# Kernel optimization log

Hardware: AMD Instinct MI355X
Metric: run time of the kernel (lower is better)

The kernel has to match this reference:

```python
import jax, jax.numpy as jnp
import numpy as np

B, S, D = 2, 1024, 768
H, HD = 12, 64
E, K, F = 8, 2, 3072
EPS = 1e-5


def _ln(x, g, b):
    mu = jnp.mean(x, -1, keepdims=True)
    var = jnp.mean(jnp.square(x - mu), -1, keepdims=True)
    return (x - mu) * jax.lax.rsqrt(var + EPS) * g + b


def setup_inputs() -> dict:
    key = jax.random.key(0)
    ks = jax.random.split(key, 12)
    s = lambda k, shape, sc: jax.random.normal(k, shape, jnp.float32) * sc
    return {
        "hidden_states": s(ks[0], (B, S, D), 1.0),
        "ln1_g": jnp.ones((D,), jnp.float32), "ln1_b": jnp.zeros((D,), jnp.float32),
        "w_attn": s(ks[1], (D, 3 * D), 0.02), "b_attn": jnp.zeros((3 * D,), jnp.float32),
        "w_attnproj": s(ks[2], (D, D), 0.02), "b_attnproj": jnp.zeros((D,), jnp.float32),
        "ln2_g": jnp.ones((D,), jnp.float32), "ln2_b": jnp.zeros((D,), jnp.float32),
        "w_router": s(ks[3], (E, D), 0.01),
        "w_fc": s(ks[4], (E, D, F), 0.02 / E), "b_fc": jnp.zeros((E, F), jnp.float32),
        "w_proj": s(ks[5], (E, F, D), 0.02 / E), "b_proj": jnp.zeros((E, D), jnp.float32),
    }


def reference(hidden_states, ln1_g, ln1_b, w_attn, b_attn, w_attnproj, b_attnproj,
              ln2_g, ln2_b, w_router, w_fc, b_fc, w_proj, b_proj):
    # --- attention sub-block (GPT-2 style, causal) ---
    residual = hidden_states
    x = _ln(hidden_states, ln1_g, ln1_b)
    qkv = x @ w_attn + b_attn                         # [B,S,3D]
    q, k, v = jnp.split(qkv, 3, axis=-1)
    def heads(t):
        return t.reshape(B, S, H, HD).transpose(0, 2, 1, 3)  # [B,H,S,HD]
    q, k, v = heads(q), heads(k), heads(v)
    scores = jnp.einsum("bhqd,bhkd->bhqk", q, k) / np.sqrt(HD).astype(np.float32)
    causal = jnp.tril(jnp.ones((S, S), bool))
    scores = jnp.where(causal, scores, jnp.finfo(scores.dtype).min)
    attn = jax.nn.softmax(scores, axis=-1)
    ctx = jnp.einsum("bhqk,bhkd->bhqd", attn, v)
    ctx = ctx.transpose(0, 2, 1, 3).reshape(B, S, D)
    attn_out = ctx @ w_attnproj + b_attnproj
    hs = attn_out + residual

    # --- MoE FFN sub-block ---
    residual = hs
    x2 = _ln(hs, ln2_g, ln2_b)
    logits = x2 @ w_router.T                          # [B,S,E]
    probs = jax.nn.softmax(logits, axis=-1)
    top_w, top_idx = jax.lax.top_k(probs, K)          # [B,S,K]
    top_w = top_w / jnp.sum(top_w, -1, keepdims=True)
    gates = jnp.sum(jax.nn.one_hot(top_idx, E, dtype=x2.dtype) * top_w[..., None], axis=2)  # [B,S,E]
    h = jax.nn.gelu(jnp.einsum("bsd,edf->bsef", x2, w_fc) + b_fc, approximate=False)
    y = jnp.einsum("bsef,efd->bsed", h, w_proj) + b_proj
    moe_out = jnp.einsum("bse,bsed->bsd", gates, y)
    return moe_out + residual
```

## Files before the change

### kernel.cpp

```cpp
#include <hip/hip_runtime.h>
#include <hip/hip_bf16.h>
#include <math.h>

#define NB 2
#define SEQ 1024
#define DM 768
#define NHEAD 12
#define HDIM 64
#define NEXP 8
#define FF 3072
#define NTOK (NB*SEQ)
#define TDIM (3*DM)
#define LNEPS 1e-5f
#define NSLOT (NTOK*2)

typedef __attribute__((ext_vector_type(8))) short v8s;
typedef __attribute__((ext_vector_type(4))) float v4f;

#define GLDS16(src, dst) \
    __builtin_amdgcn_global_load_lds((const __attribute__((address_space(1))) unsigned int*)(src), \
                                     (__attribute__((address_space(3))) unsigned int*)(dst), 16, 0, 0)

#define BARF() do { asm volatile("" ::: "memory"); __builtin_amdgcn_s_barrier(); asm volatile("" ::: "memory"); } while(0)
#define WAITV(n) asm volatile("s_waitcnt vmcnt(" #n ")" ::: "memory")

static __device__ __forceinline__ float bf2f(unsigned short u){
    return __uint_as_float(((unsigned)u) << 16);
}
static __device__ __forceinline__ unsigned short f2bf(float f){
    unsigned u = __float_as_uint(f);
    u += 0x7fffu + ((u >> 16) & 1u);
    return (unsigned short)(u >> 16);
}
static __device__ __forceinline__ float gelu_exact(float x){
    return 0.5f * x * (1.0f + erff(x * 0.70710678118654752440f));
}

__global__ __launch_bounds__(256) void tconv_kernel(const float* __restrict__ in,
                                                    unsigned short* __restrict__ out,
                                                    int R, int C){
    __shared__ float T[32][33];
    size_t base = (size_t)blockIdx.z * R * C;
    int c0 = blockIdx.x * 32, r0 = blockIdx.y * 32;
    int t = threadIdx.x;
    int tr = t >> 3, tc4 = (t & 7) * 4;
    float4 v = *(const float4*)&in[base + (size_t)(r0 + tr) * C + c0 + tc4];
    T[tr][tc4+0] = v.x; T[tr][tc4+1] = v.y; T[tr][tc4+2] = v.z; T[tr][tc4+3] = v.w;
    __syncthreads();
    int oc = t >> 3, or4 = (t & 7) * 4;
    ushort4 o;
    o.x = f2bf(T[or4+0][oc]); o.y = f2bf(T[or4+1][oc]);
    o.z = f2bf(T[or4+2][oc]); o.w = f2bf(T[or4+3][oc]);
    *(ushort4*)&out[base + (size_t)(c0 + oc) * R + r0 + or4] = o;
}

__global__ __launch_bounds__(256) void ln_b(const float* __restrict__ in,
                                            const float* __restrict__ g,
                                            const float* __restrict__ b,
                                            unsigned short* __restrict__ outb){
    int t = blockIdx.x;
    const float* row = in + (size_t)t * DM;
    int tid = threadIdx.x;
    float v0 = row[tid], v1 = row[tid + 256], v2 = row[tid + 512];
    float s  = v0 + v1 + v2;
    float ss = v0*v0 + v1*v1 + v2*v2;
    for (int off = 32; off; off >>= 1){
        s  += __shfl_down(s, off);
        ss += __shfl_down(ss, off);
    }
    __shared__ float ls[4], lss[4];
    int wid = tid >> 6, lane = tid & 63;
    if (lane == 0){ ls[wid] = s; lss[wid] = ss; }
    __syncthreads();
    if (tid == 0){
        float a = ls[0] + ls[1] + ls[2] + ls[3];
        float c = lss[0] + lss[1] + lss[2] + lss[3];
        float mu = a / (float)DM;
        float var = c / (float)DM - mu * mu;
        ls[0] = mu; lss[0] = rsqrtf(var + LNEPS);
    }
    __syncthreads();
    float mu = ls[0], rs = lss[0];
    unsigned short* obrow = outb + (size_t)t * DM;
    obrow[tid]     = f2bf((v0 - mu) * rs * g[tid]       + b[tid]);
    obrow[tid+256] = f2bf((v1 - mu) * rs * g[tid + 256] + b[tid + 256]);
    obrow[tid+512] = f2bf((v2 - mu) * rs * g[tid + 512] + b[tid + 512]);
}

__global__ __launch_bounds__(256) void ln_router(const float* __restrict__ in,
                                                 const float* __restrict__ g,
                                                 const float* __restrict__ b,
                                                 const float* __restrict__ wr,
                                                 unsigned short* __restrict__ outb,
                                                 int* __restrict__ cnt,
                                                 int* __restrict__ expTok,
                                                 int* __restrict__ tokE,
                                                 int* __restrict__ tokPos,
                                                 float* __restrict__ tokGate){
    int t = blockIdx.x;
    const float* row = in + (size_t)t * DM;
    int tid = threadIdx.x;
    float v0 = row[tid], v1 = row[tid + 256], v2 = row[tid + 512];
    float s  = v0 + v1 + v2;
    float ss = v0*v0 + v1*v1 + v2*v2;
    for (int off = 32; off; off >>= 1){
        s  += __shfl_down(s, off);
        ss += __shfl_down(ss, off);
    }
    __shared__ float ls[4], lss[4];
    __shared__ float wsum[4][NEXP];
    int wid = tid >> 6, lane = tid & 63;
    if (lane == 0){ ls[wid] = s; lss[wid] = ss; }
    __syncthreads();
    if (tid == 0){
        float a = ls[0] + ls[1] + ls[2] + ls[3];
        float c = lss[0] + lss[1] + lss[2] + lss[3];
        float mu = a / (float)DM;
        float var = c / (float)DM - mu * mu;
        ls[0] = mu; lss[0] = rsqrtf(var + LNEPS);
    }
    __syncthreads();
    float mu = ls[0], rs = lss[0];
    float o0 = (v0 - mu) * rs * g[tid]       + b[tid];
    float o1 = (v1 - mu) * rs * g[tid + 256] + b[tid + 256];
    float o2 = (v2 - mu) * rs * g[tid + 512] + b[tid + 512];
    unsigned short* obrow = outb + (size_t)t * DM;
    obrow[tid] = f2bf(o0); obrow[tid+256] = f2bf(o1); obrow[tid+512] = f2bf(o2);
    float p[NEXP];
    #pragma unroll
    for (int e = 0; e < NEXP; e++)
        p[e] = o0*wr[e*DM + tid] + o1*wr[e*DM + tid + 256] + o2*wr[e*DM + tid + 512];
    #pragma unroll
    for (int e = 0; e < NEXP; e++)
        for (int off = 32; off; off >>= 1) p[e] += __shfl_down(p[e], off);
    if (lane == 0){
        #pragma unroll
        for (int e = 0; e < NEXP; e++) wsum[wid][e] = p[e];
    }
    __syncthreads();
    if (tid == 0){
        float lg[NEXP];
        #pragma unroll
        for (int e = 0; e < NEXP; e++)
            lg[e] = wsum[0][e] + wsum[1][e] + wsum[2][e] + wsum[3][e];
        int i0 = 0; float m0 = lg[0];
        #pragma unroll
        for (int e = 1; e < NEXP; e++) if (lg[e] > m0){ m0 = lg[e]; i0 = e; }
        int i1 = -1; float m1 = -INFINITY;
        #pragma unroll
        for (int e = 0; e < NEXP; e++) if (e != i0 && lg[e] > m1){ m1 = lg[e]; i1 = e; }
        float mx = fmaxf(m0, m1);
        float e0 = __expf(m0 - mx), e1 = __expf(m1 - mx);
        float inv = 1.0f / (e0 + e1);
        int p0 = atomicAdd(&cnt[i0], 1);
        int p1 = atomicAdd(&cnt[i1], 1);
        expTok[i0*NTOK + p0] = t;
        expTok[i1*NTOK + p1] = t;
        tokE[t*2]   = i0; tokE[t*2+1]   = i1;
        tokPos[t*2] = p0; tokPos[t*2+1] = p1;
        tokGate[t*2]   = e0 * inv;
        tokGate[t*2+1] = e1 * inv;
    }
}

__global__ __launch_bounds__(256) void mm_qkv(const unsigned short* __restrict__ Ab,
                                              const unsigned short* __restrict__ Bb,
                                              const float* __restrict__ bias,
                                              unsigned short* __restrict__ Qb,
                                              unsigned short* __restrict__ Kb,
                                              unsigned short* __restrict__ Vt){
    __shared__ __align__(16) unsigned short As[4][64*32];
    __shared__ __align__(16) unsigned short Bs[4][128*32];
    int bm = blockIdx.y * 64, bn = blockIdx.x * 128;
    int tid = threadIdx.x, wave = tid >> 6, lane = tid & 63;
    int quad = lane >> 4, l15 = lane & 15;
    int wm = wave >> 1, wn = wave & 1;
    int lrow = lane >> 2, lchunk = (lane & 3) * 8;
    const unsigned short* aS  = Ab + (size_t)(bm +      wave*16 + lrow) * DM + lchunk;
    const unsigned short* bS0 = Bb + (size_t)(bn +      wave*16 + lrow) * DM + lchunk;
    const unsigned short* bS1 = Bb + (size_t)(bn + 64 + wave*16 + lrow) * DM + lchunk;
    v4f acc[2][4];
    #pragma unroll
    for (int i = 0; i < 2; i++)
        #pragma unroll
        for (int j = 0; j < 4; j++) acc[i][j] = (v4f){0.f,0.f,0.f,0.f};

#define QKV_STAGE(buf, kt) do { int kb = (kt)*32; \
    GLDS16(aS  + kb, &As[buf][(wave*16)*32]); \
    GLDS16(bS0 + kb, &Bs[buf][(     wave*16)*32]); \
    GLDS16(bS1 + kb, &Bs[buf][(64 + wave*16)*32]); \
} while(0)
#define QKV_COMP(buf) do { \
    v8s a[2], bfr[4]; \
    _Pragma("unroll") \
    for (int i = 0; i < 2; i++) a[i] = *(const v8s*)&As[buf][(wm*32 + i*16 + l15)*32 + quad*8]; \
    _Pragma("unroll") \
    for (int i = 0; i < 4; i++) bfr[i] = *(const v8s*)&Bs[buf][(wn*64 + i*16 + l15)*32 + quad*8]; \
    _Pragma("unroll") \
    for (int mi = 0; mi < 2; mi++) \
        _Pragma("unroll") \
        for (int ni = 0; ni < 4; ni++) \
            acc[mi][ni] = __builtin_amdgcn_mfma_f32_16x16x32_bf16(a[mi], bfr[ni], acc[mi][ni], 0, 0, 0); \
} while(0)

    const int NK = DM/32;
    QKV_STAGE(0, 0); QKV_STAGE(1, 1); QKV_STAGE(2, 2);
    #pragma unroll 1
    for (int kt = 0; kt < NK; kt++){
        int rem = NK - kt;
        if (rem > 3){ QKV_STAGE((kt+3)&3, kt+3); WAITV(9); }
        else if (rem == 3){ WAITV(6); }
        else if (rem == 2){ WAITV(3); }
        else { WAITV(0); }
        BARF();
        QKV_COMP(kt&3);
        BARF();
    }
    int btyp = bn / DM;
    #pragma unroll
    for (int ni = 0; ni < 4; ni++){
        int n = bn + wn*64 + ni*16 + l15;
        float bb = bias[n];
        int hd = n % DM; int h = hd >> 6; int d = hd & 63;
        #pragma unroll
        for (int mi = 0; mi < 2; mi++){
            int m = bm + wm*32 + mi*16 + quad*4;
            int b = m >> 10, sd = m & 1023;
            size_t bhbase = (size_t)(b*NHEAD + h);
            if (btyp == 0){
                #pragma unroll
                for (int r = 0; r < 4; r++)
                    Qb[(bhbase*SEQ + sd + r)*HDIM + d] = f2bf((acc[mi][ni][r] + bb) * 0.125f);
            } else if (btyp == 1){
                #pragma unroll
                for (int r = 0; r < 4; r++)
                    Kb[(bhbase*SEQ + sd + r)*HDIM + d] = f2bf(acc[mi][ni][r] + bb);
            } else {
                ushort4 o;
                o.x = f2bf(acc[mi][ni][0] + bb); o.y = f2bf(acc[mi][ni][1] + bb);
                o.z = f2bf(acc[mi][ni][2] + bb); o.w = f2bf(acc[mi][ni][3] + bb);
                *(ushort4*)&Vt[(bhbase*HDIM + d)*SEQ + sd] = o;
            }
        }
    }
}

__global__ __launch_bounds__(64) void fattn(const unsigned short* __restrict__ Qb,
                                            const unsigned short* __restrict__ Kb,
                                            const unsigned short* __restrict__ Vt,
                                            unsigned short* __restrict__ ctxb){
    int bh = blockIdx.x >> 5;
    int q0 = (31 - (blockIdx.x & 31)) * 32;
    int h = bh % NHEAD, b = bh / NHEAD;
    int lane = threadIdx.x;
    int quad = lane >> 4, l15 = lane & 15;

    __shared__ __align__(16) unsigned short Plds[32*32];

    const unsigned short* qp = Qb + ((size_t)bh*SEQ + q0 + l15) * HDIM + quad*8;
    v8s qa00 = *(const v8s*)qp;
    v8s qa01 = *(const v8s*)(qp + 32);
    v8s qa10 = *(const v8s*)(qp + 16*HDIM);
    v8s qa11 = *(const v8s*)(qp + 16*HDIM + 32);

    v4f o[2][4];
    #pragma unroll
    for (int i = 0; i < 2; i++)
        #pragma unroll
        for (int j = 0; j < 4; j++) o[i][j] = (v4f){0.f,0.f,0.f,0.f};
    float mrow[2][4], lrow[2][4];
    #pragma unroll
    for (int i = 0; i < 2; i++)
        #pragma unroll
        for (int r = 0; r < 4; r++){ mrow[i][r] = -1e30f; lrow[i][r] = 0.f; }

    int nch = (q0 >> 5) + 1;
    for (int ch = 0; ch < nch; ch++){
        int kt = ch * 32;
        const unsigned short* kp = Kb + ((size_t)bh*SEQ + kt + l15) * HDIM + quad*8;
        v8s k00 = *(const v8s*)kp;
        v8s k01 = *(const v8s*)(kp + 32);
        v8s k10 = *(const v8s*)(kp + 16*HDIM);
        v8s k11 = *(const v8s*)(kp + 16*HDIM + 32);
        v4f s00 = {0,0,0,0}, s01 = {0,0,0,0}, s10 = {0,0,0,0}, s11 = {0,0,0,0};
        s00 = __builtin_amdgcn_mfma_f32_16x16x32_bf16(qa00, k00, s00, 0, 0, 0);
        s00 = __builtin_amdgcn_mfma_f32_16x16x32_bf16(qa01, k01, s00, 0, 0, 0);
        s01 = __builtin_amdgcn_mfma_f32_16x16x32_bf16(qa00, k10, s01, 0, 0, 0);
        s01 = __builtin_amdgcn_mfma_f32_16x16x32_bf16(qa01, k11, s01, 0, 0, 0);
        s10 = __builtin_amdgcn_mfma_f32_16x16x32_bf16(qa10, k00, s10, 0, 0, 0);
        s10 = __builtin_amdgcn_mfma_f32_16x16x32_bf16(qa11, k01, s10, 0, 0, 0);
        s11 = __builtin_amdgcn_mfma_f32_16x16x32_bf16(qa10, k10, s11, 0, 0, 0);
        s11 = __builtin_amdgcn_mfma_f32_16x16x32_bf16(qa11, k11, s11, 0, 0, 0);

        int key0 = kt + l15, key1 = kt + 16 + l15;
        float alpha[2][4];
        #pragma unroll
        for (int mi = 0; mi < 2; mi++){
            #pragma unroll
            for (int r = 0; r < 4; r++){
                int qrow = q0 + mi*16 + quad*4 + r;
                float sv0 = mi ? s10[r] : s00[r];
                float sv1 = mi ? s11[r] : s01[r];
                float v0 = (key0 <= qrow) ? sv0 : -1e30f;
                float v1 = (key1 <= qrow) ? sv1 : -1e30f;
                float mx = fmaxf(v0, v1);
                mx = fmaxf(mx, __shfl_xor(mx, 1));
                mx = fmaxf(mx, __shfl_xor(mx, 2));
                mx = fmaxf(mx, __shfl_xor(mx, 4));
                mx = fmaxf(mx, __shfl_xor(mx, 8));
                float mn = fmaxf(mrow[mi][r], mx);
                alpha[mi][r] = __expf(mrow[mi][r] - mn);
                float p0 = __expf(v0 - mn);
                float p1 = __expf(v1 - mn);
                float ps = p0 + p1;
                ps += __shfl_xor(ps, 1);
                ps += __shfl_xor(ps, 2);
                ps += __shfl_xor(ps, 4);
                ps += __shfl_xor(ps, 8);
                lrow[mi][r] = lrow[mi][r] * alpha[mi][r] + ps;
                mrow[mi][r] = mn;
                Plds[(mi*16 + quad*4 + r)*32 + l15]      = f2bf(p0);
                Plds[(mi*16 + quad*4 + r)*32 + 16 + l15] = f2bf(p1);
            }
        }
        #pragma unroll
        for (int mi = 0; mi < 2; mi++)
            #pragma unroll
            for (int df = 0; df < 4; df++)
                #pragma unroll
                for (int r = 0; r < 4; r++)
                    o[mi][df][r] *= alpha[mi][r];
        __syncthreads();
        v8s pa0 = *(const v8s*)&Plds[l15*32 + quad*8];
        v8s pa1 = *(const v8s*)&Plds[(16 + l15)*32 + quad*8];
        const unsigned short* vp = Vt + ((size_t)bh*HDIM + l15) * SEQ + kt + quad*8;
        #pragma unroll
        for (int df = 0; df < 4; df++){
            v8s vb = *(const v8s*)(vp + df*16*SEQ);
            o[0][df] = __builtin_amdgcn_mfma_f32_16x16x32_bf16(pa0, vb, o[0][df], 0, 0, 0);
            o[1][df] = __builtin_amdgcn_mfma_f32_16x16x32_bf16(pa1, vb, o[1][df], 0, 0, 0);
        }
        __syncthreads();
    }
    #pragma unroll
    for (int mi = 0; mi < 2; mi++){
        #pragma unroll
        for (int r = 0; r < 4; r++){
            float inv = 1.0f / lrow[mi][r];
            size_t orow = (size_t)(b*SEQ + q0 + mi*16 + quad*4 + r) * DM + h*HDIM;
            #pragma unroll
            for (int df = 0; df < 4; df++)
                ctxb[orow + df*16 + l15] = f2bf(o[mi][df][r] * inv);
        }
    }
}

__global__ __launch_bounds__(256) void mm_attnproj(const unsigned short* __restrict__ Ab,
                                                   const unsigned short* __restrict__ Bb,
                                                   const float* __restrict__ bias,
                                                   const float* __restrict__ res,
                                                   float* __restrict__ C){
    __shared__ __align__(16) unsigned short As[4][64*32];
    __shared__ __align__(16) unsigned short Bs[4][64*32];
    int bm = blockIdx.y * 64, bn = blockIdx.x * 64;
    int tid = threadIdx.x, wave = tid >> 6, lane = tid & 63;
    int quad = lane >> 4, l15 = lane & 15;
    int wm = wave >> 1, wn = wave & 1;
    int lrow = lane >> 2, lchunk = (lane & 3) * 8;
    const unsigned short* aS = Ab + (size_t)(bm + wave*16 + lrow) * DM + lchunk;
    const unsigned short* bS = Bb + (size_t)(bn + wave*16 + lrow) * DM + lchunk;
    v4f acc[2][2];
    #pragma unroll
    for (int i = 0; i < 2; i++)
        #pragma unroll
        for (int j = 0; j < 2; j++) acc[i][j] = (v4f){0.f,0.f,0.f,0.f};

#define AP_STAGE(buf, kt) do { int kb = (kt)*32; \
    GLDS16(aS + kb, &As[buf][(wave*16)*32]); \
    GLDS16(bS + kb, &Bs[buf][(wave*16)*32]); \
} while(0)
#define AP_COMP(buf) do { \
    v8s a[2], bfr[2]; \
    _Pragma("unroll") \
    for (int i = 0; i < 2; i++){ \
        a[i]   = *(const v8s*)&As[buf][(wm*32 + i*16 + l15)*32 + quad*8]; \
        bfr[i] = *(const v8s*)&Bs[buf][(wn*32 + i*16 + l15)*32 + quad*8]; \
    } \
    _Pragma("unroll") \
    for (int mi = 0; mi < 2; mi++) \
        _Pragma("unroll") \
        for (int ni = 0; ni < 2; ni++) \
            acc[mi][ni] = __builtin_amdgcn_mfma_f32_16x16x32_bf16(a[mi], bfr[ni], acc[mi][ni], 0, 0, 0); \
} while(0)

    const int NK = DM/32;
    AP_STAGE(0, 0); AP_STAGE(1, 1); AP_STAGE(2, 2);
    #pragma unroll 1
    for (int kt = 0; kt < NK; kt++){
        int rem = NK - kt;
        if (rem > 3){ AP_STAGE((kt+3)&3, kt+3); WAITV(6); }
        else if (rem == 3){ WAITV(4); }
        else if (rem == 2){ WAITV(2); }
        else { WAITV(0); }
        BARF();
        AP_COMP(kt&3);
        BARF();
    }
    #pragma unroll
    for (int ni = 0; ni < 2; ni++){
        int n = bn + wn*32 + ni*16 + l15;
        float bb = bias[n];
        #pragma unroll
        for (int mi = 0; mi < 2; mi++){
            int m = bm + wm*32 + mi*16 + quad*4;
            #pragma unroll
            for (int r = 0; r < 4; r++)
                C[(size_t)(m + r) * DM + n] = acc[mi][ni][r] + bb + res[(size_t)(m + r) * DM + n];
        }
    }
}

__global__ __launch_bounds__(256) void mm_fc(const unsigned short* __restrict__ Xb,
                                             const unsigned short* __restrict__ Wb,
                                             const float* __restrict__ bfc,
                                             const int* __restrict__ expTok,
                                             const int* __restrict__ cnt,
                                             const int* __restrict__ offE,
                                             unsigned short* __restrict__ H){
    int e = blockIdx.z, tile = blockIdx.y;
    int c = cnt[e];
    int rows = c - tile * 64;
    if (rows <= 0) return;
    __shared__ __align__(16) unsigned short As[4][64*32];
    __shared__ __align__(16) unsigned short Bs[4][128*32];
    __shared__ int toks[64];
    int bn = blockIdx.x * 128;
    int tid = threadIdx.x, wave = tid >> 6, lane = tid & 63;
    if (tid < 64){
        int idx = tile * 64 + tid;
        if (idx >= c) idx = c - 1;
        toks[tid] = expTok[e * NTOK + idx];
    }
    __syncthreads();
    int quad = lane >> 4, l15 = lane & 15;
    int wm = wave >> 1, wn = wave & 1;
    int lrow = lane >> 2, lchunk = (lane & 3) * 8;
    int tok0 = toks[wave*16 + lrow];
    const unsigned short* Be = Wb + (size_t)e * FF * DM;
    const unsigned short* aS  = Xb + (size_t)tok0 * DM + lchunk;
    const unsigned short* bS0 = Be + (size_t)(bn +      wave*16 + lrow) * DM + lchunk;
    const unsigned short* bS1 = Be + (size_t)(bn + 64 + wave*16 + lrow) * DM + lchunk;
    v4f acc[2][4];
    #pragma unroll
    for (int i = 0; i < 2; i++)
        #pragma unroll
        for (int j = 0; j < 4; j++) acc[i][j] = (v4f){0.f,0.f,0.f,0.f};

#define FC_STAGE(buf, kt) do { int kb = (kt)*32; \
    GLDS16(aS  + kb, &As[buf][(wave*16)*32]); \
    GLDS16(bS0 + kb, &Bs[buf][(     wave*16)*32]); \
    GLDS16(bS1 + kb, &Bs[buf][(64 + wave*16)*32]); \
} while(0)
#define FC_COMP(buf) do { \
    v8s a[2], bfr[4]; \
    _Pragma("unroll") \
    for (int i = 0; i < 2; i++) a[i] = *(const v8s*)&As[buf][(wm*32 + i*16 + l15)*32 + quad*8]; \
    _Pragma("unroll") \
    for (int i = 0; i < 4; i++) bfr[i] = *(const v8s*)&Bs[buf][(wn*64 + i*16 + l15)*32 + quad*8]; \
    _Pragma("unroll") \
    for (int mi = 0; mi < 2; mi++) \
        _Pragma("unroll") \
        for (int ni = 0; ni < 4; ni++) \
            acc[mi][ni] = __builtin_amdgcn_mfma_f32_16x16x32_bf16(a[mi], bfr[ni], acc[mi][ni], 0, 0, 0); \
} while(0)

    const int NK = DM/32;
    FC_STAGE(0, 0); FC_STAGE(1, 1); FC_STAGE(2, 2);
    #pragma unroll 1
    for (int kt = 0; kt < NK; kt++){
        int rem = NK - kt;
        if (rem > 3){ FC_STAGE((kt+3)&3, kt+3); WAITV(9); }
        else if (rem == 3){ WAITV(6); }
        else if (rem == 2){ WAITV(3); }
        else { WAITV(0); }
        BARF();
        FC_COMP(kt&3);
        BARF();
    }
    int slot0 = offE[e] + tile * 64;
    #pragma unroll
    for (int ni = 0; ni < 4; ni++){
        int n = bn + wn*64 + ni*16 + l15;
        float bb = bfc[(size_t)e * FF + n];
        #pragma unroll
        for (int mi = 0; mi < 2; mi++){
            int ml = wm*32 + mi*16 + quad*4;
            #pragma unroll
            for (int r = 0; r < 4; r++)
                if (ml + r < rows)
                    H[(size_t)(slot0 + ml + r) * FF + n] = f2bf(gelu_exact(acc[mi][ni][r] + bb));
        }
    }
}

__global__ __launch_bounds__(256) void mm_proj(const unsigned short* __restrict__ H,
                                               const unsigned short* __restrict__ Wb,
                                               const int* __restrict__ cnt,
                                               const int* __restrict__ offE,
                                               float* __restrict__ Yp){
    int e = blockIdx.z, tile = blockIdx.y;
    int c = cnt[e];
    int rows = c - tile * 64;
    if (rows <= 0) return;
    int sk = blockIdx.x & 1;
    int bn = (blockIdx.x >> 1) * 128;
    __shared__ __align__(16) unsigned short As[4][64*32];
    __shared__ __align__(16) unsigned short Bs[4][128*32];
    int tid = threadIdx.x, wave = tid >> 6, lane = tid & 63;
    int quad = lane >> 4, l15 = lane & 15;
    int wm = wave >> 1, wn = wave & 1;
    int slot0 = offE[e] + tile * 64;
    int lrow = lane >> 2, lchunk = (lane & 3) * 8;
    int arow = wave*16 + lrow;
    int arl = arow < rows ? arow : rows - 1;
    const unsigned short* Be = Wb + (size_t)e * DM * FF;
    const unsigned short* aS  = H  + (size_t)(slot0 + arl) * FF + sk*1536 + lchunk;
    const unsigned short* bS0 = Be + (size_t)(bn +      wave*16 + lrow) * FF + sk*1536 + lchunk;
    const unsigned short* bS1 = Be + (size_t)(bn + 64 + wave*16 + lrow) * FF + sk*1536 + lchunk;
    v4f acc[2][4];
    #pragma unroll
    for (int i = 0; i < 2; i++)
        #pragma unroll
        for (int j = 0; j < 4; j++) acc[i][j] = (v4f){0.f,0.f,0.f,0.f};

#define PJ_STAGE(buf, kt) do { int kb = (kt)*32; \
    GLDS16(aS  + kb, &As[buf][(wave*16)*32]); \
    GLDS16(bS0 + kb, &Bs[buf][(     wave*16)*32]); \
    GLDS16(bS1 + kb, &Bs[buf][(64 + wave*16)*32]); \
} while(0)
#define PJ_COMP(buf) do { \
    v8s a[2], bfr[4]; \
    _Pragma("unroll") \
    for (int i = 0; i < 2; i++) a[i] = *(const v8s*)&As[buf][(wm*32 + i*16 + l15)*32 + quad*8]; \
    _Pragma("unroll") \
    for (int i = 0; i < 4; i++) bfr[i] = *(const v8s*)&Bs[buf][(wn*64 + i*16 + l15)*32 + quad*8]; \
    _Pragma("unroll") \
    for (int mi = 0; mi < 2; mi++) \
        _Pragma("unroll") \
        for (int ni = 0; ni < 4; ni++) \
            acc[mi][ni] = __builtin_amdgcn_mfma_f32_16x16x32_bf16(a[mi], bfr[ni], acc[mi][ni], 0, 0, 0); \
} while(0)

    const int NK = 1536/32;
    PJ_STAGE(0, 0); PJ_STAGE(1, 1); PJ_STAGE(2, 2);
    #pragma unroll 1
    for (int kt = 0; kt < NK; kt++){
        int rem = NK - kt;
        if (rem > 3){ PJ_STAGE((kt+3)&3, kt+3); WAITV(9); }
        else if (rem == 3){ WAITV(6); }
        else if (rem == 2){ WAITV(3); }
        else { WAITV(0); }
        BARF();
        PJ_COMP(kt&3);
        BARF();
    }
    float* Yo = Yp + (size_t)sk * NSLOT * DM;
    #pragma unroll
    for (int ni = 0; ni < 4; ni++){
        int n = bn + wn*64 + ni*16 + l15;
        #pragma unroll
        for (int mi = 0; mi < 2; mi++){
            int ml = wm*32 + mi*16 + quad*4;
            #pragma unroll
            for (int r = 0; r < 4; r++)
                if (ml + r < rows)
                    Yo[(size_t)(slot0 + ml + r) * DM + n] = acc[mi][ni][r];
        }
    }
}

__global__ void offsets_kernel(const int* __restrict__ cnt, int* __restrict__ offE){
    if (threadIdx.x == 0 && blockIdx.x == 0){
        int a = 0;
        for (int e = 0; e < NEXP; e++){ offE[e] = a; a += cnt[e]; }
    }
}

__global__ __launch_bounds__(256) void combine_kernel(const float* __restrict__ hs,
                                                      const float* __restrict__ Yp,
                                                      const float* __restrict__ bproj,
                                                      const int* __restrict__ tokE,
                                                      const int* __restrict__ tokPos,
                                                      const float* __restrict__ tokGate,
                                                      const int* __restrict__ offE,
                                                      float* __restrict__ out){
    int t = blockIdx.x;
    int e0 = tokE[t*2], e1 = tokE[t*2+1];
    int s0 = offE[e0] + tokPos[t*2];
    int s1 = offE[e1] + tokPos[t*2+1];
    float g0 = tokGate[t*2], g1 = tokGate[t*2+1];
    const float* y0a = Yp + (size_t)s0 * DM;
    const float* y0b = Yp + (size_t)NSLOT * DM + (size_t)s0 * DM;
    const float* y1a = Yp + (size_t)s1 * DM;
    const float* y1b = Yp + (size_t)NSLOT * DM + (size_t)s1 * DM;
    const float* b0 = bproj + (size_t)e0 * DM;
    const float* b1 = bproj + (size_t)e1 * DM;
    const float* hr = hs + (size_t)t * DM;
    float* orow = out + (size_t)t * DM;
    for (int d = threadIdx.x; d < DM; d += 256){
        orow[d] = hr[d] + g0 * (y0a[d] + y0b[d] + b0[d]) + g1 * (y1a[d] + y1b[d] + b1[d]);
    }
}

extern "C" void kernel_launch(void* const* d_in, const int* in_sizes, int n_in,
                              void* d_out, int out_size, void* d_ws, size_t ws_size,
                              hipStream_t stream){
    (void)in_sizes; (void)n_in; (void)out_size; (void)ws_size;
    const float* hidden  = (const float*)d_in[0];
    const float* ln1_g   = (const float*)d_in[1];
    const float* ln1_b   = (const float*)d_in[2];
    const float* w_attn  = (const float*)d_in[3];
    const float* b_attn  = (const float*)d_in[4];
    const float* w_aproj = (const float*)d_in[5];
    const float* b_aproj = (const float*)d_in[6];
    const float* ln2_g   = (const float*)d_in[7];
    const float* ln2_b   = (const float*)d_in[8];
    const float* w_rout  = (const float*)d_in[9];
    const float* w_fc    = (const float*)d_in[10];
    const float* b_fc    = (const float*)d_in[11];
    const float* w_proj  = (const float*)d_in[12];
    const float* b_proj  = (const float*)d_in[13];
    float* out = (float*)d_out;

    char* ws = (char*)d_ws;
    float*          hs   = (float*)(ws + 0);
    unsigned short* xb   = (unsigned short*)(ws + 6291456);
    unsigned short* Qb   = (unsigned short*)(ws + 9437184);
    unsigned short* Kb   = (unsigned short*)(ws + 12582912);
    unsigned short* Vt   = (unsigned short*)(ws + 15728640);
    unsigned short* ctxb = (unsigned short*)(ws + 18874368);
    unsigned short* Wab  = (unsigned short*)(ws + 22020096);
    unsigned short* Wapb = (unsigned short*)(ws + 25559040);
    unsigned short* H    = (unsigned short*)(ws + 9437184);
    unsigned short* Wfcb = (unsigned short*)(ws + 34603008);
    unsigned short* Wprb = (unsigned short*)(ws + 72351744);
    float*          Yp   = (float*)(ws + 34603008);
    char* rt = ws + 110100480;
    int* cnt      = (int*)(rt + 0);
    int* offE     = (int*)(rt + 64);
    int* expTok   = (int*)(rt + 128);
    int* tokE     = (int*)(rt + 128 + 65536);
    int* tokPos   = (int*)(rt + 128 + 81920);
    float* tokGate= (float*)(rt + 128 + 98304);

    hipMemsetAsync(cnt, 0, NEXP * sizeof(int), stream);

    tconv_kernel<<<dim3(TDIM/32, DM/32, 1), 256, 0, stream>>>(w_attn, Wab, DM, TDIM);
    tconv_kernel<<<dim3(DM/32, DM/32, 1), 256, 0, stream>>>(w_aproj, Wapb, DM, DM);
    tconv_kernel<<<dim3(FF/32, DM/32, NEXP), 256, 0, stream>>>(w_fc, Wfcb, DM, FF);
    tconv_kernel<<<dim3(DM/32, FF/32, NEXP), 256, 0, stream>>>(w_proj, Wprb, FF, DM);

    ln_b<<<NTOK, 256, 0, stream>>>(hidden, ln1_g, ln1_b, xb);
    mm_qkv<<<dim3(TDIM/128, NTOK/64), 256, 0, stream>>>(xb, Wab, b_attn, Qb, Kb, Vt);
    fattn<<<NB*NHEAD*32, 64, 0, stream>>>(Qb, Kb, Vt, ctxb);
    mm_attnproj<<<dim3(DM/64, NTOK/64), 256, 0, stream>>>(ctxb, Wapb, b_aproj, hidden, hs);
    ln_router<<<NTOK, 256, 0, stream>>>(hs, ln2_g, ln2_b, w_rout, xb,
                                        cnt, expTok, tokE, tokPos, tokGate);
    offsets_kernel<<<1, 64, 0, stream>>>(cnt, offE);
    mm_fc<<<dim3(FF/128, NTOK/64, NEXP), 256, 0, stream>>>(xb, Wfcb, b_fc, expTok, cnt, offE, H);
    mm_proj<<<dim3((DM/128)*2, NTOK/64, NEXP), 256, 0, stream>>>(H, Wprb, cnt, offE, Yp);
    combine_kernel<<<NTOK, 256, 0, stream>>>(hs, Yp, b_proj, tokE, tokPos, tokGate, offE, out);
}
```

Measured before the change: 493.0 us.

## Shrink QKV and proj GEMM tiles to 64x64 and use double buffering

The QKV and MoE down-projection GEMMs go from 64x128 to 64x64 output tiles, which doubles their grid size. All three GEMMs (QKV, FC, proj) drop the 4-stage global-to-LDS prefetch pipeline for 2-stage double buffering. The goal is to cut LDS use per block so more blocks fit on each CU, and to expose more parallelism in the smaller GEMMs. The cost is shallower latency hiding and less operand reuse per tile.

```diff
diff --git a/kernel.cpp b/kernel.cpp
--- a/kernel.cpp
+++ b/kernel.cpp
@@ -169,57 +169,53 @@
                                               unsigned short* __restrict__ Qb,
                                               unsigned short* __restrict__ Kb,
                                               unsigned short* __restrict__ Vt){
-    __shared__ __align__(16) unsigned short As[4][64*32];
-    __shared__ __align__(16) unsigned short Bs[4][128*32];
-    int bm = blockIdx.y * 64, bn = blockIdx.x * 128;
+    __shared__ __align__(16) unsigned short As[2][64*32];
+    __shared__ __align__(16) unsigned short Bs[2][64*32];
+    int bm = blockIdx.y * 64, bn = blockIdx.x * 64;
     int tid = threadIdx.x, wave = tid >> 6, lane = tid & 63;
     int quad = lane >> 4, l15 = lane & 15;
     int wm = wave >> 1, wn = wave & 1;
-    int lrow = lane >> 2, lchunk = (lane & 3) * 8;
-    const unsigned short* aS  = Ab + (size_t)(bm +      wave*16 + lrow) * DM + lchunk;
-    const unsigned short* bS0 = Bb + (size_t)(bn +      wave*16 + lrow) * DM + lchunk;
-    const unsigned short* bS1 = Bb + (size_t)(bn + 64 + wave*16 + lrow) * DM + lchunk;
-    v4f acc[2][4];
+    int arow = tid >> 2, achunk = (tid & 3) * 8;
+    const unsigned short* aS = Ab + (size_t)(bm + arow) * DM + achunk;
+    const unsigned short* bS = Bb + (size_t)(bn + arow) * DM + achunk;
+    v4f acc[2][2];
     #pragma unroll
     for (int i = 0; i < 2; i++)
         #pragma unroll
-        for (int j = 0; j < 4; j++) acc[i][j] = (v4f){0.f,0.f,0.f,0.f};
+        for (int j = 0; j < 2; j++) acc[i][j] = (v4f){0.f,0.f,0.f,0.f};
 
 #define QKV_STAGE(buf, kt) do { int kb = (kt)*32; \
-    GLDS16(aS  + kb, &As[buf][(wave*16)*32]); \
-    GLDS16(bS0 + kb, &Bs[buf][(     wave*16)*32]); \
-    GLDS16(bS1 + kb, &Bs[buf][(64 + wave*16)*32]); \
+    GLDS16(aS + kb, &As[buf][(wave*16)*32]); \
+    GLDS16(bS + kb, &Bs[buf][(wave*16)*32]); \
 } while(0)
 #define QKV_COMP(buf) do { \
-    v8s a[2], bfr[4]; \
-    _Pragma("unroll") \
-    for (int i = 0; i < 2; i++) a[i] = *(const v8s*)&As[buf][(wm*32 + i*16 + l15)*32 + quad*8]; \
-    _Pragma("unroll") \
-    for (int i = 0; i < 4; i++) bfr[i] = *(const v8s*)&Bs[buf][(wn*64 + i*16 + l15)*32 + quad*8]; \
+    v8s a[2], bfr[2]; \
+    _Pragma("unroll") \
+    for (int i = 0; i < 2; i++){ \
+        a[i]   = *(const v8s*)&As[buf][(wm*32 + i*16 + l15)*32 + quad*8]; \
+        bfr[i] = *(const v8s*)&Bs[buf][(wn*32 + i*16 + l15)*32 + quad*8]; \
+    } \
     _Pragma("unroll") \
     for (int mi = 0; mi < 2; mi++) \
         _Pragma("unroll") \
-        for (int ni = 0; ni < 4; ni++) \
+        for (int ni = 0; ni < 2; ni++) \
             acc[mi][ni] = __builtin_amdgcn_mfma_f32_16x16x32_bf16(a[mi], bfr[ni], acc[mi][ni], 0, 0, 0); \
 } while(0)
 
     const int NK = DM/32;
-    QKV_STAGE(0, 0); QKV_STAGE(1, 1); QKV_STAGE(2, 2);
+    QKV_STAGE(0, 0);
     #pragma unroll 1
     for (int kt = 0; kt < NK; kt++){
-        int rem = NK - kt;
-        if (rem > 3){ QKV_STAGE((kt+3)&3, kt+3); WAITV(9); }
-        else if (rem == 3){ WAITV(6); }
-        else if (rem == 2){ WAITV(3); }
-        else { WAITV(0); }
-        BARF();
-        QKV_COMP(kt&3);
+        if (NK - kt > 1){ QKV_STAGE((kt+1)&1, kt+1); WAITV(2); }
+        else            { WAITV(0); }
+        BARF();
+        QKV_COMP(kt&1);
         BARF();
     }
     int btyp = bn / DM;
     #pragma unroll
-    for (int ni = 0; ni < 4; ni++){
-        int n = bn + wn*64 + ni*16 + l15;
+    for (int ni = 0; ni < 2; ni++){
+        int n = bn + wn*32 + ni*16 + l15;
         float bb = bias[n];
         int hd = n % DM; int h = hd >> 6; int d = hd & 63;
         #pragma unroll
@@ -431,8 +427,8 @@
     int c = cnt[e];
     int rows = c - tile * 64;
     if (rows <= 0) return;
-    __shared__ __align__(16) unsigned short As[4][64*32];
-    __shared__ __align__(16) unsigned short Bs[4][128*32];
+    __shared__ __align__(16) unsigned short As[2][64*32];
+    __shared__ __align__(16) unsigned short Bs[2][128*32];
     __shared__ int toks[64];
     int bn = blockIdx.x * 128;
     int tid = threadIdx.x, wave = tid >> 6, lane = tid & 63;
@@ -475,16 +471,13 @@
 } while(0)
 
     const int NK = DM/32;
-    FC_STAGE(0, 0); FC_STAGE(1, 1); FC_STAGE(2, 2);
+    FC_STAGE(0, 0);
     #pragma unroll 1
     for (int kt = 0; kt < NK; kt++){
-        int rem = NK - kt;
-        if (rem > 3){ FC_STAGE((kt+3)&3, kt+3); WAITV(9); }
-        else if (rem == 3){ WAITV(6); }
-        else if (rem == 2){ WAITV(3); }
-        else { WAITV(0); }
-        BARF();
-        FC_COMP(kt&3);
+        if (NK - kt > 1){ FC_STAGE((kt+1)&1, kt+1); WAITV(3); }
+        else            { WAITV(0); }
+        BARF();
+        FC_COMP(kt&1);
         BARF();
     }
     int slot0 = offE[e] + tile * 64;
@@ -513,61 +506,56 @@
     int rows = c - tile * 64;
     if (rows <= 0) return;
     int sk = blockIdx.x & 1;
-    int bn = (blockIdx.x >> 1) * 128;
-    __shared__ __align__(16) unsigned short As[4][64*32];
-    __shared__ __align__(16) unsigned short Bs[4][128*32];
+    int bn = (blockIdx.x >> 1) * 64;
+    __shared__ __align__(16) unsigned short As[2][64*32];
+    __shared__ __align__(16) unsigned short Bs[2][64*32];
     int tid = threadIdx.x, wave = tid >> 6, lane = tid & 63;
     int quad = lane >> 4, l15 = lane & 15;
     int wm = wave >> 1, wn = wave & 1;
     int slot0 = offE[e] + tile * 64;
-    int lrow = lane >> 2, lchunk = (lane & 3) * 8;
-    int arow = wave*16 + lrow;
+    int arow = tid >> 2, achunk = (tid & 3) * 8;
     int arl = arow < rows ? arow : rows - 1;
     const unsigned short* Be = Wb + (size_t)e * DM * FF;
-    const unsigned short* aS  = H  + (size_t)(slot0 + arl) * FF + sk*1536 + lchunk;
-    const unsigned short* bS0 = Be + (size_t)(bn +      wave*16 + lrow) * FF + sk*1536 + lchunk;
-    const unsigned short* bS1 = Be + (size_t)(bn + 64 + wave*16 + lrow) * FF + sk*1536 + lchunk;
-    v4f acc[2][4];
+    const unsigned short* aS = H  + (size_t)(slot0 + arl) * FF + sk*1536 + achunk;
+    const unsigned short* bS = Be + (size_t)(bn + arow) * FF + sk*1536 + achunk;
+    v4f acc[2][2];
     #pragma unroll
     for (int i = 0; i < 2; i++)
         #pragma unroll
-        for (int j = 0; j < 4; j++) acc[i][j] = (v4f){0.f,0.f,0.f,0.f};
+        for (int j = 0; j < 2; j++) acc[i][j] = (v4f){0.f,0.f,0.f,0.f};
 
 #define PJ_STAGE(buf, kt) do { int kb = (kt)*32; \
-    GLDS16(aS  + kb, &As[buf][(wave*16)*32]); \
-    GLDS16(bS0 + kb, &Bs[buf][(     wave*16)*32]); \
-    GLDS16(bS1 + kb, &Bs[buf][(64 + wave*16)*32]); \
+    GLDS16(aS + kb, &As[buf][(wave*16)*32]); \
+    GLDS16(bS + kb, &Bs[buf][(wave*16)*32]); \
 } while(0)
 #define PJ_COMP(buf) do { \
-    v8s a[2], bfr[4]; \
-    _Pragma("unroll") \
-    for (int i = 0; i < 2; i++) a[i] = *(const v8s*)&As[buf][(wm*32 + i*16 + l15)*32 + quad*8]; \
-    _Pragma("unroll") \
-    for (int i = 0; i < 4; i++) bfr[i] = *(const v8s*)&Bs[buf][(wn*64 + i*16 + l15)*32 + quad*8]; \
+    v8s a[2], bfr[2]; \
+    _Pragma("unroll") \
+    for (int i = 0; i < 2; i++){ \
+        a[i]   = *(const v8s*)&As[buf][(wm*32 + i*16 + l15)*32 + quad*8]; \
+        bfr[i] = *(const v8s*)&Bs[buf][(wn*32 + i*16 + l15)*32 + quad*8]; \
+    } \
     _Pragma("unroll") \
     for (int mi = 0; mi < 2; mi++) \
         _Pragma("unroll") \
-        for (int ni = 0; ni < 4; ni++) \
+        for (int ni = 0; ni < 2; ni++) \
             acc[mi][ni] = __builtin_amdgcn_mfma_f32_16x16x32_bf16(a[mi], bfr[ni], acc[mi][ni], 0, 0, 0); \
 } while(0)
 
     const int NK = 1536/32;
-    PJ_STAGE(0, 0); PJ_STAGE(1, 1); PJ_STAGE(2, 2);
+    PJ_STAGE(0, 0);
     #pragma unroll 1
     for (int kt = 0; kt < NK; kt++){
-        int rem = NK - kt;
-        if (rem > 3){ PJ_STAGE((kt+3)&3, kt+3); WAITV(9); }
-        else if (rem == 3){ WAITV(6); }
-        else if (rem == 2){ WAITV(3); }
-        else { WAITV(0); }
-        BARF();
-        PJ_COMP(kt&3);
+        if (NK - kt > 1){ PJ_STAGE((kt+1)&1, kt+1); WAITV(2); }
+        else            { WAITV(0); }
+        BARF();
+        PJ_COMP(kt&1);
         BARF();
     }
     float* Yo = Yp + (size_t)sk * NSLOT * DM;
     #pragma unroll
-    for (int ni = 0; ni < 4; ni++){
-        int n = bn + wn*64 + ni*16 + l15;
+    for (int ni = 0; ni < 2; ni++){
+        int n = bn + wn*32 + ni*16 + l15;
         #pragma unroll
         for (int mi = 0; mi < 2; mi++){
             int ml = wm*32 + mi*16 + quad*4;
@@ -661,13 +649,13 @@
     tconv_kernel<<<dim3(DM/32, FF/32, NEXP), 256, 0, stream>>>(w_proj, Wprb, FF, DM);
 
     ln_b<<<NTOK, 256, 0, stream>>>(hidden, ln1_g, ln1_b, xb);
-    mm_qkv<<<dim3(TDIM/128, NTOK/64), 256, 0, stream>>>(xb, Wab, b_attn, Qb, Kb, Vt);
+    mm_qkv<<<dim3(TDIM/64, NTOK/64), 256, 0, stream>>>(xb, Wab, b_attn, Qb, Kb, Vt);
     fattn<<<NB*NHEAD*32, 64, 0, stream>>>(Qb, Kb, Vt, ctxb);
     mm_attnproj<<<dim3(DM/64, NTOK/64), 256, 0, stream>>>(ctxb, Wapb, b_aproj, hidden, hs);
     ln_router<<<NTOK, 256, 0, stream>>>(hs, ln2_g, ln2_b, w_rout, xb,
                                         cnt, expTok, tokE, tokPos, tokGate);
     offsets_kernel<<<1, 64, 0, stream>>>(cnt, offE);
     mm_fc<<<dim3(FF/128, NTOK/64, NEXP), 256, 0, stream>>>(xb, Wfcb, b_fc, expTok, cnt, offE, H);
-    mm_proj<<<dim3((DM/128)*2, NTOK/64, NEXP), 256, 0, stream>>>(H, Wprb, cnt, offE, Yp);
+    mm_proj<<<dim3((DM/64)*2, NTOK/64, NEXP), 256, 0, stream>>>(H, Wprb, cnt, offE, Yp);
     combine_kernel<<<NTOK, 256, 0, stream>>>(hs, Yp, b_proj, tokE, tokPos, tokGate, offE, out);
 }
```

After: 487.7 us. No clear change (-1.1%).
